# Performance work log

Measured on AMD Instinct MI355X. Metric: run time of the kernel, lower is better.

The kernel has to match this reference:

```python
import jax, jax.numpy as jnp
import numpy as np

ZDIM, NF, H, S, B = 64, 32, 256, 256, 1024


def setup_inputs() -> dict:
    key = jax.random.key(0)
    ks = jax.random.split(key, 8)
    def w(k, shape, fan):
        return (jax.random.normal(k, shape, jnp.float32) / np.sqrt(fan)).astype(jnp.float32)
    return {
        "z": jax.random.normal(ks[0], (B, ZDIM), jnp.float32),
        "W_lat": w(ks[1], (2 * H, ZDIM), ZDIM),
        "b_lat": jnp.zeros((2 * H,), jnp.float32),
        "W_ih": w(ks[2], (4 * H, NF), NF),
        "b_ih": jnp.zeros((4 * H,), jnp.float32),
        "W_hh": w(ks[3], (4 * H, H), H),
        "b_hh": jnp.zeros((4 * H,), jnp.float32),
        "W_out": w(ks[4], (NF, H), H),
        "b_out": jnp.zeros((NF,), jnp.float32),
        "W_sig": w(ks[5], (NF, H * S), H * S),
        "b_sig": jnp.zeros((NF,), jnp.float32),
    }


def reference(z, W_lat, b_lat, W_ih, b_ih, W_hh, b_hh, W_out, b_out, W_sig, b_sig):
    # from_latent: split into initial hidden / cell state
    hc = z @ W_lat.T + b_lat                      # [B, 2H]
    h, c = hc[:, :H], hc[:, H:]
    x = jnp.zeros((z.shape[0], NF), z.dtype)      # initial LSTM input
    bias = b_ih + b_hh                            # fold both LSTM biases

    def step(carry, _):
        h, c, x = carry
        g = x @ W_ih.T + h @ W_hh.T + bias        # [B, 4H]; torch gate order i,f,g,o
        i, f, gg, o = jnp.split(g, 4, axis=-1)
        c = jax.nn.sigmoid(f) * c + jax.nn.sigmoid(i) * jnp.tanh(gg)
        h = jax.nn.sigmoid(o) * jnp.tanh(c)
        x_next = jnp.tanh(h) @ W_out.T + b_out    # activation(Tanh) then from_lstm
        return (h, c, x_next), (h, x_next)

    _, (hs, mus) = jax.lax.scan(step, (h, c, x), None, length=S)
    # mus: [S, B, NF] -> mu: [B, NF, S]
    mu = jnp.transpose(mus, (1, 2, 0))
    # hs: [S, B, H] -> [B, H, S] -> flatten hidden-major, matching torch permute+reshape
    xs = jnp.transpose(hs, (1, 2, 0)).reshape(-1, H * S)
    sigma = jax.nn.softplus(xs @ W_sig.T + b_sig)[:, :, None]   # [B, NF, 1]
    return (mu, sigma)
```

## Files before the change

kernel.cpp:

```cpp
#include <hip/hip_runtime.h>

#define NF 32
#define HDIM 256
#define SLEN 256
#define BATCH 1024

typedef float f32x4 __attribute__((ext_vector_type(4)));
typedef __bf16 bf16x8 __attribute__((ext_vector_type(8)));
typedef unsigned int u32x4 __attribute__((ext_vector_type(4)));
typedef unsigned short u16;

#define MFMA __builtin_amdgcn_mfma_f32_16x16x32_bf16

#define WHH_O 0
#define WIH_O 32768
#define WOUT_O 36864
#define WLAT_O 37888
#define PREP1_N 41984
#define WT_BYTE (1u << 20)
#define HST_BYTE (8u << 20)

__device__ __forceinline__ u16 f2bf(float x) {
  union { float f; unsigned int u; } v; v.f = x;
  return (u16)((v.u + 0x7FFFu + ((v.u >> 16) & 1u)) >> 16);
}
__device__ __forceinline__ unsigned int pk2(float a, float b) {
  return (unsigned int)f2bf(a) | ((unsigned int)f2bf(b) << 16);
}
__device__ __forceinline__ float sigf(float x) {
  return __fdividef(1.0f, 1.0f + __expf(-x));
}
__device__ __forceinline__ float tanhf_(float x) {
  return 1.0f - __fdividef(2.0f, __expf(2.0f * x) + 1.0f);
}

__global__ void prep_weights(const float* __restrict__ Whh, const float* __restrict__ Wih,
                             const float* __restrict__ Wout, const float* __restrict__ Wlat,
                             uint4* __restrict__ ws) {
  int i = blockIdx.x * 256 + threadIdx.x;
  if (i >= PREP1_N) return;
  int l = i & 63;
  int c16 = l & 15, g4 = l >> 4;
  const float* src;
  if (i < WIH_O) {
    int t = (i >> 6) & 7, j = i >> 9;
    src = Whh + (j * 16 + c16) * 256 + t * 32 + 8 * g4;
  } else if (i < WOUT_O) {
    int ii = i - WIH_O;
    int j = ii >> 6;
    src = Wih + (j * 16 + c16) * 32 + 8 * g4;
  } else if (i < WLAT_O) {
    int ii = i - WOUT_O;
    int t = (ii >> 6) & 7, j = ii >> 9;
    src = Wout + (j * 16 + c16) * 256 + t * 32 + 8 * g4;
  } else {
    int ii = i - WLAT_O;
    int t = (ii >> 6) & 1, j = ii >> 7;
    src = Wlat + (j * 16 + c16) * 64 + t * 32 + 8 * g4;
  }
  uint4 P;
  P.x = pk2(src[0], src[1]);
  P.y = pk2(src[2], src[3]);
  P.z = pk2(src[4], src[5]);
  P.w = pk2(src[6], src[7]);
  ws[i] = P;
}

__global__ void prep_wt(const float* __restrict__ Wsig, unsigned short* __restrict__ Wt) {
  __shared__ float tile[32][257];
  int f = blockIdx.x >> 3, hb = blockIdx.x & 7;
  int tid = threadIdx.x;
  const float* src = Wsig + f * (HDIM * SLEN) + hb * 32 * 256;
#pragma unroll
  for (int i = 0; i < 32; ++i) tile[i][tid] = src[i * 256 + tid];
  __syncthreads();
  int s = tid;
  unsigned short tmp[32];
#pragma unroll
  for (int h = 0; h < 32; ++h) tmp[h] = f2bf(tile[h][s]);
  uint4* dst = (uint4*)(Wt + f * 65536 + s * 256 + hb * 32);
  const uint4* tsrc = (const uint4*)tmp;
#pragma unroll
  for (int j = 0; j < 4; ++j) dst[j] = tsrc[j];
}

__global__ __launch_bounds__(512, 2) void lstm_scan(
    const float* __restrict__ z, const float* __restrict__ b_lat,
    const float* __restrict__ b_ih, const float* __restrict__ b_hh,
    const float* __restrict__ b_out,
    const uint4* __restrict__ ws, unsigned short* __restrict__ hst,
    float* __restrict__ out) {
  __shared__ __align__(16) uint4 whhl[8192];
  __shared__ __align__(16) u16 hbuf[2][16][256];
  __shared__ __align__(16) u16 thbuf[16][256];
  __shared__ __align__(16) u16 xbuf[2][16][32];

  const int tid = threadIdx.x, w = tid >> 6, l = tid & 63;
  const int c16 = l & 15, g4 = l >> 4, r0 = g4 * 4;
  const int wg = blockIdx.x;
  const int swz = (c16 & 7) << 3;

  for (int i = tid; i < 8192; i += 512) {
    int l_ = i & 63, kt = (i >> 6) & 7, qq = (i >> 9) & 1, w_ = i >> 10;
    whhl[i] = ws[WHH_O + (((4 + qq) * 8 + w_) * 8 + kt) * 64 + l_];
  }

  u32x4 wp[3][8];
#pragma unroll
  for (int qi = 0; qi < 3; ++qi)
#pragma unroll
    for (int kt = 0; kt < 8; ++kt)
      wp[qi][kt] = __builtin_bit_cast(u32x4, ws[WHH_O + ((qi * 8 + w) * 8 + kt) * 64 + l]);
#pragma unroll
  for (int qi = 0; qi < 3; ++qi)
#pragma unroll
    for (int kt = 0; kt < 8; ++kt)
      asm volatile("" : "+v"(wp[qi][kt]));

  float biasv[8];
#pragma unroll
  for (int q = 0; q < 8; ++q) {
    int n = (q * 8 + w) * 16 + c16;
    biasv[q] = b_ih[n] + b_hh[n];
  }
  float bo = (w < 2) ? b_out[w * 16 + c16] : 0.f;

  for (int idx = tid; idx < 1024; idx += 512)
    thbuf[idx >> 6][idx & 63] = f2bf(z[(wg * 16 + (idx >> 6)) * 64 + (idx & 63)]);
  xbuf[0][tid >> 5][tid & 31] = 0;
  __syncthreads();

  float cst[2][4];
  {
    bf16x8 za0 = *reinterpret_cast<const bf16x8*>(&thbuf[c16][8 * g4]);
    bf16x8 za1 = *reinterpret_cast<const bf16x8*>(&thbuf[c16][32 + 8 * g4]);
    f32x4 a2[4];
#pragma unroll
    for (int q2 = 0; q2 < 4; ++q2) {
      int j = q2 * 8 + w;
      float bl = b_lat[j * 16 + c16];
      f32x4 a = {bl, bl, bl, bl};
      a = MFMA(za0, *reinterpret_cast<const bf16x8*>(ws + WLAT_O + (j * 2 + 0) * 64 + l), a, 0, 0, 0);
      a = MFMA(za1, *reinterpret_cast<const bf16x8*>(ws + WLAT_O + (j * 2 + 1) * 64 + l), a, 0, 0, 0);
      a2[q2] = a;
    }
#pragma unroll
    for (int q2 = 0; q2 < 2; ++q2) {
      int col = q2 * 128 + w * 16 + c16;
#pragma unroll
      for (int v = 0; v < 4; ++v) {
        int rr = r0 + v;
        hbuf[0][rr][col ^ ((rr & 7) << 3)] = f2bf(a2[q2][v]);
      }
    }
#pragma unroll
    for (int p = 0; p < 2; ++p)
#pragma unroll
      for (int v = 0; v < 4; ++v) cst[p][v] = a2[2 + p][v];
  }
  __syncthreads();

  const uint4* bs3 = ws + WHH_O + ((3 * 8 + w) * 8) * 64 + l;
  const uint4* bs6 = ws + WHH_O + ((6 * 8 + w) * 8) * 64 + l;
  const uint4* bs7 = ws + WHH_O + ((7 * 8 + w) * 8) * 64 + l;

  for (int s = 0; s < SLEN; ++s) {
    const int pb = s & 1;
    uint4 pf[12];
#pragma unroll
    for (int kt = 0; kt < 4; ++kt) {
      pf[kt * 3 + 0] = bs3[kt * 64];
      pf[kt * 3 + 1] = bs6[kt * 64];
      pf[kt * 3 + 2] = bs7[kt * 64];
    }
    f32x4 acc[8];
#pragma unroll
    for (int q = 0; q < 8; ++q) acc[q] = (f32x4){biasv[q], biasv[q], biasv[q], biasv[q]};
#pragma unroll
    for (int kt = 0; kt < 8; ++kt) {
      bf16x8 afr = *reinterpret_cast<const bf16x8*>(&hbuf[pb][c16][(kt * 32 + 8 * g4) ^ swz]);
      acc[0] = MFMA(afr, __builtin_bit_cast(bf16x8, wp[0][kt]), acc[0], 0, 0, 0);
      acc[1] = MFMA(afr, __builtin_bit_cast(bf16x8, wp[1][kt]), acc[1], 0, 0, 0);
      acc[2] = MFMA(afr, __builtin_bit_cast(bf16x8, wp[2][kt]), acc[2], 0, 0, 0);
      acc[4] = MFMA(afr, *reinterpret_cast<const bf16x8*>(&whhl[((w * 2 + 0) * 8 + kt) * 64 + l]), acc[4], 0, 0, 0);
      acc[5] = MFMA(afr, *reinterpret_cast<const bf16x8*>(&whhl[((w * 2 + 1) * 8 + kt) * 64 + l]), acc[5], 0, 0, 0);
    }
    bf16x8 wihv[8];
#pragma unroll
    for (int q = 0; q < 8; ++q)
      wihv[q] = *reinterpret_cast<const bf16x8*>(ws + WIH_O + (q * 8 + w) * 64 + l);
#pragma unroll
    for (int kt = 0; kt < 4; ++kt) {
      bf16x8 afr = *reinterpret_cast<const bf16x8*>(&hbuf[pb][c16][(kt * 32 + 8 * g4) ^ swz]);
      acc[3] = MFMA(afr, __builtin_bit_cast(bf16x8, pf[kt * 3 + 0]), acc[3], 0, 0, 0);
      acc[6] = MFMA(afr, __builtin_bit_cast(bf16x8, pf[kt * 3 + 1]), acc[6], 0, 0, 0);
      acc[7] = MFMA(afr, __builtin_bit_cast(bf16x8, pf[kt * 3 + 2]), acc[7], 0, 0, 0);
      pf[kt * 3 + 0] = bs3[(4 + kt) * 64];
      pf[kt * 3 + 1] = bs6[(4 + kt) * 64];
      pf[kt * 3 + 2] = bs7[(4 + kt) * 64];
    }
#pragma unroll
    for (int kt = 4; kt < 8; ++kt) {
      bf16x8 afr = *reinterpret_cast<const bf16x8*>(&hbuf[pb][c16][(kt * 32 + 8 * g4) ^ swz]);
      acc[3] = MFMA(afr, __builtin_bit_cast(bf16x8, pf[(kt - 4) * 3 + 0]), acc[3], 0, 0, 0);
      acc[6] = MFMA(afr, __builtin_bit_cast(bf16x8, pf[(kt - 4) * 3 + 1]), acc[6], 0, 0, 0);
      acc[7] = MFMA(afr, __builtin_bit_cast(bf16x8, pf[(kt - 4) * 3 + 2]), acc[7], 0, 0, 0);
    }
    bf16x8 xfr = *reinterpret_cast<const bf16x8*>(&xbuf[pb][c16][8 * g4]);
#pragma unroll
    for (int q = 0; q < 8; ++q) acc[q] = MFMA(xfr, wihv[q], acc[q], 0, 0, 0);

#pragma unroll
    for (int p = 0; p < 2; ++p) {
      const int hcol = p * 128 + w * 16 + c16;
#pragma unroll
      for (int v = 0; v < 4; ++v) {
        float iv = acc[0 + p][v];
        float fv = acc[2 + p][v];
        float gv = acc[4 + p][v];
        float ov = acc[6 + p][v];
        float cc = sigf(fv) * cst[p][v] + sigf(iv) * tanhf_(gv);
        cst[p][v] = cc;
        float hh = sigf(ov) * tanhf_(cc);
        float th = tanhf_(hh);
        int rr = r0 + v;
        int sc = hcol ^ ((rr & 7) << 3);
        hbuf[pb ^ 1][rr][sc] = f2bf(hh);
        thbuf[rr][sc] = f2bf(th);
      }
    }
    __syncthreads();
    if (w < 2) {
      f32x4 xacc = {bo, bo, bo, bo};
#pragma unroll
      for (int t = 0; t < 8; ++t) {
        bf16x8 ta = *reinterpret_cast<const bf16x8*>(&thbuf[c16][(t * 32 + 8 * g4) ^ swz]);
        bf16x8 wov = *reinterpret_cast<const bf16x8*>(ws + WOUT_O + (w * 8 + t) * 64 + l);
        xacc = MFMA(ta, wov, xacc, 0, 0, 0);
      }
      const int f = w * 16 + c16;
#pragma unroll
      for (int v = 0; v < 4; ++v) {
        int rr = r0 + v;
        float xv = xacc[v];
        xbuf[pb ^ 1][rr][f] = f2bf(xv);
        out[(wg * 16 + rr) * (NF * SLEN) + f * SLEN + s] = xv;
      }
    } else if (w >= 4) {
      int t4 = tid - 256;
#pragma unroll
      for (int rep = 0; rep < 2; ++rep) {
        int task = t4 + rep * 256;
        int r = task >> 5;
        int h0 = (task & 31) * 8;
        uint4 d = *reinterpret_cast<const uint4*>(&hbuf[pb ^ 1][r][h0 ^ ((r & 7) << 3)]);
        *reinterpret_cast<uint4*>(hst + ((wg * 16 + r) << 16) + (s << 8) + h0) = d;
      }
    }
    __syncthreads();
  }
}

__global__ __launch_bounds__(512) void sigma_gemm(
    const unsigned short* __restrict__ hst, const unsigned short* __restrict__ Wt,
    const float* __restrict__ b_sig, float* __restrict__ out) {
  __shared__ float sred[8][16][32];
  const int tid = threadIdx.x;
  const int w = tid >> 6;
  const int l = tid & 63;
  const int c16 = l & 15;
  const int g4 = l >> 4;
  const int wg = blockIdx.x;

  const unsigned short* ap =
      hst + (((wg << 2) + (c16 & 3)) << 16) + ((w * 32) << 8) + (g4 << 3);
  const unsigned short* bp0 = Wt + (c16 << 16) + ((w * 32) << 8) + (g4 << 3);
  const unsigned short* bp1 = Wt + ((16 + c16) << 16) + ((w * 32) << 8) + (g4 << 3);

  f32x4 a0 = {0.f, 0.f, 0.f, 0.f}, a1 = {0.f, 0.f, 0.f, 0.f};
#pragma unroll 8
  for (int kk = 0; kk < 256; ++kk) {
    int off = ((kk >> 3) << 8) + ((kk & 7) << 5);
    bf16x8 av = *reinterpret_cast<const bf16x8*>(ap + off);
    a0 = MFMA(av, *reinterpret_cast<const bf16x8*>(bp0 + off), a0, 0, 0, 0);
    a1 = MFMA(av, *reinterpret_cast<const bf16x8*>(bp1 + off), a1, 0, 0, 0);
  }
#pragma unroll
  for (int v = 0; v < 4; ++v) {
    sred[w][g4 * 4 + v][c16] = a0[v];
    sred[w][g4 * 4 + v][16 + c16] = a1[v];
  }
  __syncthreads();
  int b = tid >> 5, f = tid & 31;
  if (b < 4) {
    float acc = b_sig[f];
#pragma unroll
    for (int ww = 0; ww < 8; ++ww) acc += sred[ww][b][f];
    float sp = fmaxf(acc, 0.0f) + log1pf(__expf(-fabsf(acc)));
    out[BATCH * NF * SLEN + ((wg << 2) + b) * NF + f] = sp;
  }
}

extern "C" void kernel_launch(void* const* d_in, const int* in_sizes, int n_in,
                              void* d_out, int out_size, void* d_ws, size_t ws_size,
                              hipStream_t stream) {
  (void)in_sizes; (void)n_in; (void)out_size; (void)ws_size;
  const float* z     = (const float*)d_in[0];
  const float* W_lat = (const float*)d_in[1];
  const float* b_lat = (const float*)d_in[2];
  const float* W_ih  = (const float*)d_in[3];
  const float* b_ih  = (const float*)d_in[4];
  const float* W_hh  = (const float*)d_in[5];
  const float* b_hh  = (const float*)d_in[6];
  const float* W_out = (const float*)d_in[7];
  const float* b_out = (const float*)d_in[8];
  const float* W_sig = (const float*)d_in[9];
  const float* b_sig = (const float*)d_in[10];
  char* wsb = (char*)d_ws;
  uint4* ws = (uint4*)wsb;
  unsigned short* Wt  = (unsigned short*)(wsb + WT_BYTE);
  unsigned short* hst = (unsigned short*)(wsb + HST_BYTE);
  float* out = (float*)d_out;

  prep_weights<<<(PREP1_N + 255) / 256, 256, 0, stream>>>(W_hh, W_ih, W_out, W_lat, ws);
  prep_wt<<<256, 256, 0, stream>>>(W_sig, Wt);
  lstm_scan<<<64, 512, 0, stream>>>(z, b_lat, b_ih, b_hh, b_out, ws, hst, out);
  sigma_gemm<<<256, 512, 0, stream>>>(hst, Wt, b_sig, out);
}
```

Measured before the change: 3.485 ms.

## Split LSTM scan across 16 waves per block and buffer mu writes

The LSTM scan block grows from 512 to 1024 threads, so each wave owns one 16-column slice of every gate instead of two. The register- and LDS-resident W_hh copies are dropped, and all W_hh fragments are now streamed from global/L2 on every step. W_out fragments are hoisted into registers of the two output waves. Mu outputs are staged in shared memory and written as 16-step vectorized chunks instead of strided scalar stores each step. The trade is more parallel MFMA issue per step and fewer scattered stores, at the cost of heavy per-step global weight traffic and larger barriers.

```diff
diff --git a/kernel.cpp b/kernel.cpp
--- a/kernel.cpp
+++ b/kernel.cpp
@@ -84,180 +84,136 @@
   for (int j = 0; j < 4; ++j) dst[j] = tsrc[j];
 }
 
-__global__ __launch_bounds__(512, 2) void lstm_scan(
+__global__ __launch_bounds__(1024) void lstm_scan(
     const float* __restrict__ z, const float* __restrict__ b_lat,
     const float* __restrict__ b_ih, const float* __restrict__ b_hh,
     const float* __restrict__ b_out,
     const uint4* __restrict__ ws, unsigned short* __restrict__ hst,
     float* __restrict__ out) {
-  __shared__ __align__(16) uint4 whhl[8192];
   __shared__ __align__(16) u16 hbuf[2][16][256];
   __shared__ __align__(16) u16 thbuf[16][256];
   __shared__ __align__(16) u16 xbuf[2][16][32];
+  __shared__ __align__(16) float mubuf[16][16][32];
 
   const int tid = threadIdx.x, w = tid >> 6, l = tid & 63;
   const int c16 = l & 15, g4 = l >> 4, r0 = g4 * 4;
   const int wg = blockIdx.x;
   const int swz = (c16 & 7) << 3;
 
-  for (int i = tid; i < 8192; i += 512) {
-    int l_ = i & 63, kt = (i >> 6) & 7, qq = (i >> 9) & 1, w_ = i >> 10;
-    whhl[i] = ws[WHH_O + (((4 + qq) * 8 + w_) * 8 + kt) * 64 + l_];
-  }
-
-  u32x4 wp[3][8];
-#pragma unroll
-  for (int qi = 0; qi < 3; ++qi)
-#pragma unroll
-    for (int kt = 0; kt < 8; ++kt)
-      wp[qi][kt] = __builtin_bit_cast(u32x4, ws[WHH_O + ((qi * 8 + w) * 8 + kt) * 64 + l]);
-#pragma unroll
-  for (int qi = 0; qi < 3; ++qi)
-#pragma unroll
-    for (int kt = 0; kt < 8; ++kt)
-      asm volatile("" : "+v"(wp[qi][kt]));
-
-  float biasv[8];
-#pragma unroll
-  for (int q = 0; q < 8; ++q) {
-    int n = (q * 8 + w) * 16 + c16;
-    biasv[q] = b_ih[n] + b_hh[n];
-  }
-  float bo = (w < 2) ? b_out[w * 16 + c16] : 0.f;
-
-  for (int idx = tid; idx < 1024; idx += 512)
-    thbuf[idx >> 6][idx & 63] = f2bf(z[(wg * 16 + (idx >> 6)) * 64 + (idx & 63)]);
-  xbuf[0][tid >> 5][tid & 31] = 0;
-  __syncthreads();
-
-  float cst[2][4];
+  bf16x8 wih[4];
+  float biasv[4];
+#pragma unroll
+  for (int gi = 0; gi < 4; ++gi) {
+    int j = gi * 16 + w;
+    wih[gi] = *reinterpret_cast<const bf16x8*>(ws + WIH_O + j * 64 + l);
+    int n = j * 16 + c16;
+    biasv[gi] = b_ih[n] + b_hh[n];
+  }
+  const int jn = w - 14;
+  bf16x8 wo[8];
+  float bo = 0.f;
+  if (w >= 14) {
+#pragma unroll
+    for (int t = 0; t < 8; ++t)
+      wo[t] = *reinterpret_cast<const bf16x8*>(ws + WOUT_O + (jn * 8 + t) * 64 + l);
+    bo = b_out[jn * 16 + c16];
+  }
+
+  thbuf[tid >> 6][tid & 63] = f2bf(z[(wg * 16 + (tid >> 6)) * 64 + (tid & 63)]);
+  if (tid < 512) xbuf[0][tid >> 5][tid & 31] = 0;
+  __syncthreads();
+
+  float cst[4];
   {
     bf16x8 za0 = *reinterpret_cast<const bf16x8*>(&thbuf[c16][8 * g4]);
     bf16x8 za1 = *reinterpret_cast<const bf16x8*>(&thbuf[c16][32 + 8 * g4]);
-    f32x4 a2[4];
-#pragma unroll
-    for (int q2 = 0; q2 < 4; ++q2) {
-      int j = q2 * 8 + w;
-      float bl = b_lat[j * 16 + c16];
-      f32x4 a = {bl, bl, bl, bl};
-      a = MFMA(za0, *reinterpret_cast<const bf16x8*>(ws + WLAT_O + (j * 2 + 0) * 64 + l), a, 0, 0, 0);
-      a = MFMA(za1, *reinterpret_cast<const bf16x8*>(ws + WLAT_O + (j * 2 + 1) * 64 + l), a, 0, 0, 0);
-      a2[q2] = a;
-    }
-#pragma unroll
-    for (int q2 = 0; q2 < 2; ++q2) {
-      int col = q2 * 128 + w * 16 + c16;
-#pragma unroll
-      for (int v = 0; v < 4; ++v) {
-        int rr = r0 + v;
-        hbuf[0][rr][col ^ ((rr & 7) << 3)] = f2bf(a2[q2][v]);
-      }
-    }
-#pragma unroll
-    for (int p = 0; p < 2; ++p)
-#pragma unroll
-      for (int v = 0; v < 4; ++v) cst[p][v] = a2[2 + p][v];
-  }
-  __syncthreads();
-
-  const uint4* bs3 = ws + WHH_O + ((3 * 8 + w) * 8) * 64 + l;
-  const uint4* bs6 = ws + WHH_O + ((6 * 8 + w) * 8) * 64 + l;
-  const uint4* bs7 = ws + WHH_O + ((7 * 8 + w) * 8) * 64 + l;
+    float blh = b_lat[w * 16 + c16];
+    float blc = b_lat[256 + w * 16 + c16];
+    f32x4 ah = {blh, blh, blh, blh}, ac = {blc, blc, blc, blc};
+    ah = MFMA(za0, *reinterpret_cast<const bf16x8*>(ws + WLAT_O + (w * 2 + 0) * 64 + l), ah, 0, 0, 0);
+    ah = MFMA(za1, *reinterpret_cast<const bf16x8*>(ws + WLAT_O + (w * 2 + 1) * 64 + l), ah, 0, 0, 0);
+    ac = MFMA(za0, *reinterpret_cast<const bf16x8*>(ws + WLAT_O + ((16 + w) * 2 + 0) * 64 + l), ac, 0, 0, 0);
+    ac = MFMA(za1, *reinterpret_cast<const bf16x8*>(ws + WLAT_O + ((16 + w) * 2 + 1) * 64 + l), ac, 0, 0, 0);
+    const int hc = w * 16 + c16;
+#pragma unroll
+    for (int v = 0; v < 4; ++v) {
+      cst[v] = ac[v];
+      int rr = r0 + v;
+      hbuf[0][rr][hc ^ ((rr & 7) << 3)] = f2bf(ah[v]);
+    }
+  }
+  __syncthreads();
 
   for (int s = 0; s < SLEN; ++s) {
     const int pb = s & 1;
-    uint4 pf[12];
-#pragma unroll
-    for (int kt = 0; kt < 4; ++kt) {
-      pf[kt * 3 + 0] = bs3[kt * 64];
-      pf[kt * 3 + 1] = bs6[kt * 64];
-      pf[kt * 3 + 2] = bs7[kt * 64];
-    }
-    f32x4 acc[8];
-#pragma unroll
-    for (int q = 0; q < 8; ++q) acc[q] = (f32x4){biasv[q], biasv[q], biasv[q], biasv[q]};
-#pragma unroll
-    for (int kt = 0; kt < 8; ++kt) {
-      bf16x8 afr = *reinterpret_cast<const bf16x8*>(&hbuf[pb][c16][(kt * 32 + 8 * g4) ^ swz]);
-      acc[0] = MFMA(afr, __builtin_bit_cast(bf16x8, wp[0][kt]), acc[0], 0, 0, 0);
-      acc[1] = MFMA(afr, __builtin_bit_cast(bf16x8, wp[1][kt]), acc[1], 0, 0, 0);
-      acc[2] = MFMA(afr, __builtin_bit_cast(bf16x8, wp[2][kt]), acc[2], 0, 0, 0);
-      acc[4] = MFMA(afr, *reinterpret_cast<const bf16x8*>(&whhl[((w * 2 + 0) * 8 + kt) * 64 + l]), acc[4], 0, 0, 0);
-      acc[5] = MFMA(afr, *reinterpret_cast<const bf16x8*>(&whhl[((w * 2 + 1) * 8 + kt) * 64 + l]), acc[5], 0, 0, 0);
-    }
-    bf16x8 wihv[8];
-#pragma unroll
-    for (int q = 0; q < 8; ++q)
-      wihv[q] = *reinterpret_cast<const bf16x8*>(ws + WIH_O + (q * 8 + w) * 64 + l);
-#pragma unroll
-    for (int kt = 0; kt < 4; ++kt) {
-      bf16x8 afr = *reinterpret_cast<const bf16x8*>(&hbuf[pb][c16][(kt * 32 + 8 * g4) ^ swz]);
-      acc[3] = MFMA(afr, __builtin_bit_cast(bf16x8, pf[kt * 3 + 0]), acc[3], 0, 0, 0);
-      acc[6] = MFMA(afr, __builtin_bit_cast(bf16x8, pf[kt * 3 + 1]), acc[6], 0, 0, 0);
-      acc[7] = MFMA(afr, __builtin_bit_cast(bf16x8, pf[kt * 3 + 2]), acc[7], 0, 0, 0);
-      pf[kt * 3 + 0] = bs3[(4 + kt) * 64];
-      pf[kt * 3 + 1] = bs6[(4 + kt) * 64];
-      pf[kt * 3 + 2] = bs7[(4 + kt) * 64];
-    }
-#pragma unroll
-    for (int kt = 4; kt < 8; ++kt) {
-      bf16x8 afr = *reinterpret_cast<const bf16x8*>(&hbuf[pb][c16][(kt * 32 + 8 * g4) ^ swz]);
-      acc[3] = MFMA(afr, __builtin_bit_cast(bf16x8, pf[(kt - 4) * 3 + 0]), acc[3], 0, 0, 0);
-      acc[6] = MFMA(afr, __builtin_bit_cast(bf16x8, pf[(kt - 4) * 3 + 1]), acc[6], 0, 0, 0);
-      acc[7] = MFMA(afr, __builtin_bit_cast(bf16x8, pf[(kt - 4) * 3 + 2]), acc[7], 0, 0, 0);
-    }
+    bf16x8 afr[8];
+#pragma unroll
+    for (int kt = 0; kt < 8; ++kt)
+      afr[kt] = *reinterpret_cast<const bf16x8*>(&hbuf[pb][c16][(kt * 32 + 8 * g4) ^ swz]);
     bf16x8 xfr = *reinterpret_cast<const bf16x8*>(&xbuf[pb][c16][8 * g4]);
-#pragma unroll
-    for (int q = 0; q < 8; ++q) acc[q] = MFMA(xfr, wihv[q], acc[q], 0, 0, 0);
-
-#pragma unroll
-    for (int p = 0; p < 2; ++p) {
-      const int hcol = p * 128 + w * 16 + c16;
+    f32x4 acc[4];
+#pragma unroll
+    for (int gi = 0; gi < 4; ++gi) {
+      f32x4 a = {biasv[gi], biasv[gi], biasv[gi], biasv[gi]};
+      a = MFMA(xfr, wih[gi], a, 0, 0, 0);
+      const uint4* bp = ws + WHH_O + ((gi * 16 + w) * 8) * 64 + l;
+#pragma unroll
+      for (int kt = 0; kt < 8; ++kt)
+        a = MFMA(afr[kt], *reinterpret_cast<const bf16x8*>(bp + kt * 64), a, 0, 0, 0);
+      acc[gi] = a;
+    }
+    {
+      const int hc = w * 16 + c16;
 #pragma unroll
       for (int v = 0; v < 4; ++v) {
-        float iv = acc[0 + p][v];
-        float fv = acc[2 + p][v];
-        float gv = acc[4 + p][v];
-        float ov = acc[6 + p][v];
-        float cc = sigf(fv) * cst[p][v] + sigf(iv) * tanhf_(gv);
-        cst[p][v] = cc;
+        float iv = acc[0][v];
+        float fv = acc[1][v];
+        float gv = acc[2][v];
+        float ov = acc[3][v];
+        float cc = sigf(fv) * cst[v] + sigf(iv) * tanhf_(gv);
+        cst[v] = cc;
         float hh = sigf(ov) * tanhf_(cc);
         float th = tanhf_(hh);
         int rr = r0 + v;
-        int sc = hcol ^ ((rr & 7) << 3);
+        int sc = hc ^ ((rr & 7) << 3);
         hbuf[pb ^ 1][rr][sc] = f2bf(hh);
         thbuf[rr][sc] = f2bf(th);
       }
     }
     __syncthreads();
-    if (w < 2) {
+    if (w >= 14) {
       f32x4 xacc = {bo, bo, bo, bo};
 #pragma unroll
       for (int t = 0; t < 8; ++t) {
         bf16x8 ta = *reinterpret_cast<const bf16x8*>(&thbuf[c16][(t * 32 + 8 * g4) ^ swz]);
-        bf16x8 wov = *reinterpret_cast<const bf16x8*>(ws + WOUT_O + (w * 8 + t) * 64 + l);
-        xacc = MFMA(ta, wov, xacc, 0, 0, 0);
-      }
-      const int f = w * 16 + c16;
+        xacc = MFMA(ta, wo[t], xacc, 0, 0, 0);
+      }
+      const int f = jn * 16 + c16;
+      const int sw = s & 15;
 #pragma unroll
       for (int v = 0; v < 4; ++v) {
         int rr = r0 + v;
-        float xv = xacc[v];
-        xbuf[pb ^ 1][rr][f] = f2bf(xv);
-        out[(wg * 16 + rr) * (NF * SLEN) + f * SLEN + s] = xv;
-      }
-    } else if (w >= 4) {
-      int t4 = tid - 256;
-#pragma unroll
-      for (int rep = 0; rep < 2; ++rep) {
-        int task = t4 + rep * 256;
-        int r = task >> 5;
-        int h0 = (task & 31) * 8;
-        uint4 d = *reinterpret_cast<const uint4*>(&hbuf[pb ^ 1][r][h0 ^ ((r & 7) << 3)]);
-        *reinterpret_cast<uint4*>(hst + ((wg * 16 + r) << 16) + (s << 8) + h0) = d;
-      }
+        xbuf[pb ^ 1][rr][f] = f2bf(xacc[v]);
+        mubuf[sw][rr][f] = xacc[v];
+      }
+    } else if (w < 8) {
+      int r = tid >> 5;
+      int h0 = (tid & 31) * 8;
+      uint4 d = *reinterpret_cast<const uint4*>(&hbuf[pb ^ 1][r][h0 ^ ((r & 7) << 3)]);
+      *reinterpret_cast<uint4*>(hst + ((wg * 16 + r) << 16) + (s << 8) + h0) = d;
     }
     __syncthreads();
+    if ((s & 15) == 15 && tid < 512) {
+      int b = tid >> 5, f = tid & 31;
+      float* dst = out + ((wg * 16 + b) << 13) + (f << 8) + (s - 15);
+#pragma unroll
+      for (int j4 = 0; j4 < 4; ++j4) {
+        f32x4 vv;
+#pragma unroll
+        for (int jj = 0; jj < 4; ++jj) vv[jj] = mubuf[j4 * 4 + jj][b][f];
+        *reinterpret_cast<f32x4*>(dst + j4 * 4) = vv;
+      }
+    }
   }
 }
 
@@ -324,6 +280,6 @@
 
   prep_weights<<<(PREP1_N + 255) / 256, 256, 0, stream>>>(W_hh, W_ih, W_out, W_lat, ws);
   prep_wt<<<256, 256, 0, stream>>>(W_sig, Wt);
-  lstm_scan<<<64, 512, 0, stream>>>(z, b_lat, b_ih, b_hh, b_out, ws, hst, out);
+  lstm_scan<<<64, 1024, 0, stream>>>(z, b_lat, b_ih, b_hh, b_out, ws, hst, out);
   sigma_gemm<<<256, 512, 0, stream>>>(hst, Wt, b_sig, out);
 }
```

New measurement: 3.878 ms. +11.3%, slower.
